# Kernel optimization log

Hardware: AMD Instinct MI355X
Metric: run time of the kernel (lower is better)

The kernel has to match this reference:

```python
import jax, jax.numpy as jnp
import numpy as np


def _kernels(r):
    """Build the 8 normalized directional box kernels, shape [8,1,k,k]."""
    k = 2 * r + 1
    ones = np.ones((k, k), np.float32)
    L = ones.copy(); L[:, r + 1:] = 0
    R = ones.copy(); R[:, :r] = 0
    U = ones.copy(); U[r + 1:, :] = 0
    D = ones.copy(); D[:r, :] = 0
    NW = U.copy(); NW[:, r + 1:] = 0
    NE = U.copy(); NE[:, :r] = 0
    SW = D.copy(); SW[:, r + 1:] = 0
    SE = D.copy(); SE[:, :r] = 0
    half = np.float32((r + 1) * k)
    quad = np.float32((r + 1) ** 2)
    ker = np.stack([L / half, R / half, U / half, D / half,
                    NW / quad, NE / quad, SW / quad, SE / quad])
    return jnp.asarray(ker[:, None, :, :])  # [8,1,k,k]


def setup_inputs() -> dict:
    key = jax.random.key(0)
    im = jax.random.uniform(key, (4, 3, 1024, 1024), dtype=jnp.float32)
    return {"im": im, "radius": 7, "iteration": 3}


def reference(im, radius, iteration):
    W = _kernels(radius)                      # [8,1,k,k] constants
    b, c, h, w = im.shape
    # channels are filtered independently -> fold channel into batch
    x = im.reshape(b * c, 1, h, w)
    pad = [(radius, radius), (radius, radius)]

    def step(x, _):
        # 8 directional box means minus center pixel: [bc,8,h,w]
        d = jax.lax.conv_general_dilated(
            x, W, window_strides=(1, 1), padding=pad,
            dimension_numbers=("NCHW", "OIHW", "NCHW")) - x
        idx = jnp.argmin(jnp.abs(d), axis=1, keepdims=True)  # [bc,1,h,w]
        dm = jnp.take_along_axis(d, idx, axis=1)
        return x + dm, None

    x, _ = jax.lax.scan(step, x, None, length=iteration)
    return x.reshape(b, c, h, w)
```

## Files before the change

kernel.cpp:

```cpp
#include <hip/hip_runtime.h>

#define HH 1024
#define WW 1024
#define NIMG 12
#define OUTC 50
#define NSTRIP 21

__device__ __forceinline__ float fwd8(float a) {
  a += __shfl_down(a, 1, 64);
  a += __shfl_down(a, 2, 64);
  a += __shfl_down(a, 4, 64);
  return a;
}

__device__ __forceinline__ float load_px(const float* __restrict__ s, int ry, int cl) {
  if ((unsigned)ry < (unsigned)HH && (unsigned)cl < (unsigned)WW)
    return s[(size_t)ry * WW + cl];
  return 0.0f;
}

__device__ __forceinline__ float winner(float a, float b) {
  return (fabsf(b) < fabsf(a)) ? b : a;
}

__device__ __forceinline__ float out_px(float ua, float ub, float uc,
                                        float da, float db, float dc,
                                        float lh0, float rh0, float w0) {
  const float ih = 1.0f / 120.0f, iq = 1.0f / 64.0f;
  const float nw0 = -w0;
  const float Ls = ua + da - lh0;
  const float Rs = ub + db - rh0;
  const float Us = ua + ub - uc;
  const float Ds = da + db - dc;
  float d0 = fmaf(Ls, ih, nw0);
  float d1 = fmaf(Rs, ih, nw0);
  float d2 = fmaf(Us, ih, nw0);
  float d3 = fmaf(Ds, ih, nw0);
  float d4 = fmaf(ua, iq, nw0);
  float d5 = fmaf(ub, iq, nw0);
  float d6 = fmaf(da, iq, nw0);
  float d7 = fmaf(db, iq, nw0);
  float w01 = winner(d0, d1), w23 = winner(d2, d3);
  float w45 = winner(d4, d5), w67 = winner(d6, d7);
  float bd = winner(winner(w01, w23), winner(w45, w67));
  return w0 + bd;
}

__global__ __launch_bounds__(256, 4) void swf_step(const float* __restrict__ src,
                                                   float* __restrict__ dst) {
  const int lane = threadIdx.x & 63;
  const int wid  = threadIdx.x >> 6;
  const int cl   = blockIdx.x * OUTC - 7 + lane;
  const int y0   = (blockIdx.y * 4 + wid) * 32;
  const float* s = src + (size_t)blockIdx.z * HH * WW;
  float* d       = dst + (size_t)blockIdx.z * HH * WW;

  const int  colOut  = cl;
  const bool writeOK = (lane >= 7) && (lane <= 56) && (colOut < WW);

  float rlh[16], rrh[16], rw[16];

  #pragma unroll
  for (int j = 0; j < 15; ++j) {
    const int slot = (j + 8) & 15;
    float wc = load_px(s, y0 - 8 + j, cl);
    float f  = fwd8(wc);
    rlh[slot] = __shfl_up(f, 7, 64);
    rrh[slot] = f;
    rw [slot] = wc;
  }

  float ua = 0.f, ub = 0.f, uc = 0.f, da = 0.f, db = 0.f, dc = 0.f;
  #pragma unroll
  for (int j = 0; j < 8; ++j) {
    const int sl = (8 + j) & 15;
    ua += rlh[sl]; ub += rrh[sl]; uc += rw[sl];
  }
  #pragma unroll
  for (int j = 0; j < 8; ++j) {
    const int sl = (15 + j) & 15;
    da += rlh[sl]; db += rrh[sl]; dc += rw[sl];
  }

  float pipe[8];
  #pragma unroll
  for (int k = 0; k < 6; ++k) pipe[k] = load_px(s, y0 + 7 + k, cl);

  #pragma unroll 1
  for (int yb = 0; yb < 32; yb += 16) {
    #pragma unroll
    for (int i = 0; i < 16; i += 2) {
      const int y = y0 + yb + i;
      pipe[(i + 6) & 7] = load_px(s, y + 13, cl);
      pipe[(i + 7) & 7] = load_px(s, y + 14, cl);

      const int ls0 = (i + 7) & 15;
      const int ls1 = (i + 8) & 15;

      const float t0 = pipe[i & 7];
      const float t1 = pipe[(i + 1) & 7];
      float f0 = fwd8(t0);
      float f1 = fwd8(t1);
      float l0 = __shfl_up(f0, 7, 64);
      float l1 = __shfl_up(f1, 7, 64);

      rlh[ls0] = l0; rrh[ls0] = f0; rw[ls0] = t0;

      ua += rlh[i];   ua -= rlh[ls1];
      ub += rrh[i];   ub -= rrh[ls1];
      uc += rw [i];   uc -= rw [ls1];
      da += rlh[ls0]; da -= rlh[(i + 15) & 15];
      db += rrh[ls0]; db -= rrh[(i + 15) & 15];
      dc += rw [ls0]; dc -= rw [(i + 15) & 15];
      const float o0 = out_px(ua, ub, uc, da, db, dc, rlh[i], rrh[i], rw[i]);

      rlh[ls1] = l1; rrh[ls1] = f1; rw[ls1] = t1;

      const int i1 = i + 1;
      ua += rlh[i1];  ua -= rlh[(i1 + 8) & 15];
      ub += rrh[i1];  ub -= rrh[(i1 + 8) & 15];
      uc += rw [i1];  uc -= rw [(i1 + 8) & 15];
      da += rlh[ls1]; da -= rlh[i];
      db += rrh[ls1]; db -= rrh[i];
      dc += rw [ls1]; dc -= rw [i];
      const float o1 = out_px(ua, ub, uc, da, db, dc, rlh[i1], rrh[i1], rw[i1]);

      if (writeOK) {
        d[(size_t)y * WW + colOut]       = o0;
        d[(size_t)(y + 1) * WW + colOut] = o1;
      }
    }
  }
}

extern "C" void kernel_launch(void* const* d_in, const int* in_sizes, int n_in,
                              void* d_out, int out_size, void* d_ws, size_t ws_size,
                              hipStream_t stream) {
  const float* in = (const float*)d_in[0];
  float* out = (float*)d_out;
  float* ws  = (float*)d_ws;

  dim3 grid(NSTRIP, 8, NIMG);
  dim3 block(256);

  swf_step<<<grid, block, 0, stream>>>(in, out);
  swf_step<<<grid, block, 0, stream>>>(out, ws);
  swf_step<<<grid, block, 0, stream>>>(ws, out);
}
```

Measured before the change: 123.0 us.

## Stage block input rows in LDS via direct global-to-LDS loads

Each block now copies its 143-row by 64-column input tile (with halo) into shared memory with global_load_lds before computing, and the four waves read rows from LDS instead of issuing their own global loads. This removes the per-wave register prefetch pipe and the overlapping halo reloads between waves, so each input row is fetched from global memory once per block. In exchange the loads are front-loaded behind a full wait and barrier, so load and compute no longer overlap, and the roughly 36KB of LDS per block may limit occupancy.

```diff
diff --git a/kernel.cpp b/kernel.cpp
--- a/kernel.cpp
+++ b/kernel.cpp
@@ -5,18 +5,13 @@
 #define NIMG 12
 #define OUTC 50
 #define NSTRIP 21
+#define TROWS 143
 
 __device__ __forceinline__ float fwd8(float a) {
   a += __shfl_down(a, 1, 64);
   a += __shfl_down(a, 2, 64);
   a += __shfl_down(a, 4, 64);
   return a;
-}
-
-__device__ __forceinline__ float load_px(const float* __restrict__ s, int ry, int cl) {
-  if ((unsigned)ry < (unsigned)HH && (unsigned)cl < (unsigned)WW)
-    return s[(size_t)ry * WW + cl];
-  return 0.0f;
 }
 
 __device__ __forceinline__ float winner(float a, float b) {
@@ -51,19 +46,42 @@
   const int lane = threadIdx.x & 63;
   const int wid  = threadIdx.x >> 6;
   const int cl   = blockIdx.x * OUTC - 7 + lane;
-  const int y0   = (blockIdx.y * 4 + wid) * 32;
+  const int yb0  = blockIdx.y * 128;
+  const int y0   = yb0 + wid * 32;
   const float* s = src + (size_t)blockIdx.z * HH * WW;
   float* d       = dst + (size_t)blockIdx.z * HH * WW;
 
-  const int  colOut  = cl;
-  const bool writeOK = (lane >= 7) && (lane <= 56) && (colOut < WW);
+  const bool colOK   = ((unsigned)cl < (unsigned)WW);
+  const bool writeOK = (lane >= 7) && (lane <= 56) && colOK;
+
+  __shared__ float tile[TROWS][64];
+
+  {
+    const int clg = min(max(cl, 0), WW - 1);
+    const int rb  = wid * 36;
+    const int re  = (wid == 3) ? TROWS : rb + 36;
+    for (int r = rb; r < re; ++r) {
+      const int gr  = yb0 - 8 + r;
+      const int grc = min(max(gr, 0), HH - 1);
+      const float* gp = s + (size_t)grc * WW + clg;
+      __builtin_amdgcn_global_load_lds(
+          (const __attribute__((address_space(1))) void*)gp,
+          (__attribute__((address_space(3))) void*)&tile[r][0],
+          4, 0, 0);
+    }
+  }
+  asm volatile("s_waitcnt vmcnt(0)" ::: "memory");
+  __syncthreads();
+
+  #define TP(ry) ( ((unsigned)(ry) < (unsigned)HH && colOK) \
+                     ? tile[(ry) - yb0 + 8][lane] : 0.0f )
 
   float rlh[16], rrh[16], rw[16];
 
   #pragma unroll
   for (int j = 0; j < 15; ++j) {
     const int slot = (j + 8) & 15;
-    float wc = load_px(s, y0 - 8 + j, cl);
+    float wc = TP(y0 - 8 + j);
     float f  = fwd8(wc);
     rlh[slot] = __shfl_up(f, 7, 64);
     rrh[slot] = f;
@@ -82,23 +100,17 @@
     da += rlh[sl]; db += rrh[sl]; dc += rw[sl];
   }
 
-  float pipe[8];
-  #pragma unroll
-  for (int k = 0; k < 6; ++k) pipe[k] = load_px(s, y0 + 7 + k, cl);
-
   #pragma unroll 1
   for (int yb = 0; yb < 32; yb += 16) {
     #pragma unroll
     for (int i = 0; i < 16; i += 2) {
       const int y = y0 + yb + i;
-      pipe[(i + 6) & 7] = load_px(s, y + 13, cl);
-      pipe[(i + 7) & 7] = load_px(s, y + 14, cl);
 
       const int ls0 = (i + 7) & 15;
       const int ls1 = (i + 8) & 15;
 
-      const float t0 = pipe[i & 7];
-      const float t1 = pipe[(i + 1) & 7];
+      const float t0 = TP(y + 7);
+      const float t1 = TP(y + 8);
       float f0 = fwd8(t0);
       float f1 = fwd8(t1);
       float l0 = __shfl_up(f0, 7, 64);
@@ -126,11 +138,12 @@
       const float o1 = out_px(ua, ub, uc, da, db, dc, rlh[i1], rrh[i1], rw[i1]);
 
       if (writeOK) {
-        d[(size_t)y * WW + colOut]       = o0;
-        d[(size_t)(y + 1) * WW + colOut] = o1;
+        d[(size_t)y * WW + cl]       = o0;
+        d[(size_t)(y + 1) * WW + cl] = o1;
       }
     }
   }
+  #undef TP
 }
 
 extern "C" void kernel_launch(void* const* d_in, const int* in_sizes, int n_in,
```

Result: slower. 128.8 us (+4.7%).
